# Kernel optimization log

Measured on AMD Instinct MI355X. Metric: run time of the kernel, lower is better.

The kernel has to match this reference:

```python
import math
import jax, jax.numpy as jnp
from jax import lax
import numpy as np

L, B, S, H, N = 2, 1, 2048, 1024, 16
HN = H // N
EPS = 1e-5
SIGMA = 0.02
OUT_STD = SIGMA / math.sqrt(2.0 * L)


def gelu(x):
    # OpenAI tanh-approx gelu, matching gelu_impl
    return 0.5 * x * (1.0 + jnp.tanh(0.7978845608028654 * x * (1.0 + 0.044715 * x * x)))


def layer_norm(x, g, b):
    mu = jnp.mean(x, axis=-1, keepdims=True)
    var = jnp.mean(jnp.square(x - mu), axis=-1, keepdims=True)
    return (x - mu) / jnp.sqrt(var + EPS) * g + b


def setup_inputs() -> dict:
    key = jax.random.key(0)
    ks = jax.random.split(key, 8)
    x = jax.random.normal(ks[0], (B, S, H), dtype=jnp.float32)
    ltor_mask = jnp.tril(jnp.ones((S, S), dtype=jnp.float32))[None, None]  # [1,1,S,S]
    return {
        "hidden_states": x,
        "ltor_mask": ltor_mask,
        "ln1_g": jnp.ones((L, H), jnp.float32),
        "ln1_b": jnp.zeros((L, H), jnp.float32),
        "qkv_w": jax.random.normal(ks[1], (L, H, 3 * H), jnp.float32) * SIGMA,
        "qkv_b": jnp.zeros((L, 3 * H), jnp.float32),
        "dense_w": jax.random.normal(ks[2], (L, H, H), jnp.float32) * OUT_STD,
        "dense_b": jnp.zeros((L, H), jnp.float32),
        "ln2_g": jnp.ones((L, H), jnp.float32),
        "ln2_b": jnp.zeros((L, H), jnp.float32),
        "fc_w": jax.random.normal(ks[3], (L, H, 4 * H), jnp.float32) * SIGMA,
        "fc_b": jnp.zeros((L, 4 * H), jnp.float32),
        "proj_w": jax.random.normal(ks[4], (L, 4 * H, H), jnp.float32) * OUT_STD,
        "proj_b": jnp.zeros((L, H), jnp.float32),
        "lnf_g": jnp.ones((H,), jnp.float32),
        "lnf_b": jnp.zeros((H,), jnp.float32),
    }


def _transformer(hidden_states, ltor_mask, ln1_g, ln1_b, qkv_w, qkv_b, dense_w, dense_b,
                 ln2_g, ln2_b, fc_w, fc_b, proj_w, proj_b, lnf_g, lnf_b):
    scale = 1.0 / math.sqrt(HN)

    def step(h, p):
        g1, b1, qw, qb, dw, db, g2, b2, fw, fb, pw, pb = p
        y = layer_norm(h, g1, b1)
        qkv = y @ qw + qb                       # [B,S,3H]
        q, k, v = jnp.split(qkv, 3, axis=-1)
        # [B,S,H] -> [B,N,S,HN]
        q = q.reshape(B, S, N, HN).transpose(0, 2, 1, 3)
        k = k.reshape(B, S, N, HN).transpose(0, 2, 1, 3)
        v = v.reshape(B, S, N, HN).transpose(0, 2, 1, 3)
        scores = jnp.einsum('bnqd,bnkd->bnqk', q, k) * scale
        scores = scores * ltor_mask - 10000.0 * (1.0 - ltor_mask)
        probs = jax.nn.softmax(scores, axis=-1)
        ctx = jnp.einsum('bnqk,bnkd->bnqd', probs, v)
        ctx = ctx.transpose(0, 2, 1, 3).reshape(B, S, H)
        attn_out = ctx @ dw + db
        h2 = h + attn_out
        y2 = layer_norm(h2, g2, b2)
        mlp_out = gelu(y2 @ fw + fb) @ pw + pb
        return h2 + mlp_out, None

    params = (ln1_g, ln1_b, qkv_w, qkv_b, dense_w, dense_b,
              ln2_g, ln2_b, fc_w, fc_b, proj_w, proj_b)
    h, _ = lax.scan(step, hidden_states, params)
    return layer_norm(h, lnf_g, lnf_b)


def reference(hidden_states, ltor_mask, ln1_g, ln1_b, qkv_w, qkv_b, dense_w, dense_b,
              ln2_g, ln2_b, fc_w, fc_b, proj_w, proj_b, lnf_g, lnf_b):
    return _transformer(hidden_states, ltor_mask, ln1_g, ln1_b, qkv_w, qkv_b,
                        dense_w, dense_b, ln2_g, ln2_b, fc_w, fc_b,
                        proj_w, proj_b, lnf_g, lnf_b)
```

## Files before the change

kernel.cpp:

```cpp
#include <hip/hip_runtime.h>
#include <hip/hip_bf16.h>
#include <cstdint>
#include <cstddef>

typedef __bf16 bf16;
typedef __attribute__((ext_vector_type(4))) __bf16 bf16x4;
typedef __attribute__((ext_vector_type(8))) __bf16 bf16x8;
typedef __attribute__((ext_vector_type(4))) float floatx4;

__device__ __forceinline__ void gload16(const bf16* g, bf16* l) {
    __builtin_amdgcn_global_load_lds(
        (const __attribute__((address_space(1))) void*)g,
        (__attribute__((address_space(3))) void*)l, 16, 0, 0);
}

__global__ __launch_bounds__(256) void ln_first(const float* __restrict__ x,
                                                float* __restrict__ h,
                                                const float* __restrict__ g,
                                                const float* __restrict__ b,
                                                bf16* __restrict__ y) {
    __shared__ float red[8];
    const int row = blockIdx.x, tid = threadIdx.x;
    const size_t off = (size_t)row * 1024 + tid * 4;
    const float4 v = *(const float4*)(x + off);
    *(float4*)(h + off) = v;
    float s = v.x + v.y + v.z + v.w;
#pragma unroll
    for (int o = 32; o > 0; o >>= 1) s += __shfl_xor(s, o);
    if ((tid & 63) == 0) red[tid >> 6] = s;
    __syncthreads();
    const float mean = (red[0] + red[1] + red[2] + red[3]) * (1.f / 1024.f);
    const float d[4] = {v.x - mean, v.y - mean, v.z - mean, v.w - mean};
    float q = d[0] * d[0] + d[1] * d[1] + d[2] * d[2] + d[3] * d[3];
#pragma unroll
    for (int o = 32; o > 0; o >>= 1) q += __shfl_xor(q, o);
    if ((tid & 63) == 0) red[4 + (tid >> 6)] = q;
    __syncthreads();
    const float var = (red[4] + red[5] + red[6] + red[7]) * (1.f / 1024.f);
    const float rstd = rsqrtf(var + 1e-5f);
    const int base = tid * 4;
#pragma unroll
    for (int i = 0; i < 4; i++)
        y[off + i] = (bf16)(d[i] * rstd * g[base + i] + b[base + i]);
}

template <typename OutT, int KS>
__global__ __launch_bounds__(256) void reduce_ln(const bf16* __restrict__ part,
                                                 const float* __restrict__ bias,
                                                 float* __restrict__ h,
                                                 const float* __restrict__ g,
                                                 const float* __restrict__ b,
                                                 OutT* __restrict__ y) {
    __shared__ float red[8];
    const int row = blockIdx.x, tid = threadIdx.x;
    const int base = tid * 4;
    const size_t off = (size_t)row * 1024 + base;
    const float4 hv = *(const float4*)(h + off);
    const float4 bv = *(const float4*)(bias + base);
    float a[4] = {hv.x + bv.x, hv.y + bv.y, hv.z + bv.z, hv.w + bv.w};
#pragma unroll
    for (int z = 0; z < KS; z++) {
        bf16x4 pv = *(const bf16x4*)(part + (size_t)z * (2048 * 1024) + off);
#pragma unroll
        for (int i = 0; i < 4; i++) a[i] += (float)pv[i];
    }
    *(float4*)(h + off) = (float4){a[0], a[1], a[2], a[3]};
    float s = a[0] + a[1] + a[2] + a[3];
#pragma unroll
    for (int o = 32; o > 0; o >>= 1) s += __shfl_xor(s, o);
    if ((tid & 63) == 0) red[tid >> 6] = s;
    __syncthreads();
    const float mean = (red[0] + red[1] + red[2] + red[3]) * (1.f / 1024.f);
    const float d[4] = {a[0] - mean, a[1] - mean, a[2] - mean, a[3] - mean};
    float q = d[0] * d[0] + d[1] * d[1] + d[2] * d[2] + d[3] * d[3];
#pragma unroll
    for (int o = 32; o > 0; o >>= 1) q += __shfl_xor(q, o);
    if ((tid & 63) == 0) red[4 + (tid >> 6)] = q;
    __syncthreads();
    const float var = (red[4] + red[5] + red[6] + red[7]) * (1.f / 1024.f);
    const float rstd = rsqrtf(var + 1e-5f);
#pragma unroll
    for (int i = 0; i < 4; i++)
        y[off + i] = (OutT)(d[i] * rstd * g[base + i] + b[base + i]);
}

__global__ __launch_bounds__(256) void transpose_cvt(const float* __restrict__ in,
                                                     bf16* __restrict__ out, int K, int N) {
    __shared__ float T[64][65];
    const int k0 = blockIdx.x * 64, n0 = blockIdx.y * 64;
    {
        const int r = threadIdx.x >> 4;
        const int c4 = (threadIdx.x & 15) * 4;
#pragma unroll
        for (int j = 0; j < 4; j++) {
            float4 v = *(const float4*)&in[(size_t)(k0 + r + j * 16) * N + n0 + c4];
            T[r + j * 16][c4 + 0] = v.x; T[r + j * 16][c4 + 1] = v.y;
            T[r + j * 16][c4 + 2] = v.z; T[r + j * 16][c4 + 3] = v.w;
        }
    }
    __syncthreads();
    {
        const int rn = threadIdx.x >> 3;
        const int c8 = (threadIdx.x & 7) * 8;
#pragma unroll
        for (int j = 0; j < 2; j++) {
            bf16x8 v;
#pragma unroll
            for (int i = 0; i < 8; i++) v[i] = (bf16)T[c8 + i][rn + j * 32];
            *(bf16x8*)&out[(size_t)(n0 + rn + j * 32) * K + k0 + c8] = v;
        }
    }
}

template <int MODE>
__global__ __launch_bounds__(256) void gemm_bt64(const bf16* __restrict__ A,
                                                 const bf16* __restrict__ BT,
                                                 const float* __restrict__ bias,
                                                 bf16* __restrict__ outb,
                                                 int M, int N, int K) {
    __shared__ bf16 As[64 * 64];
    __shared__ bf16 Bs[128 * 64];
    const int tid = threadIdx.x;
    const int w = tid >> 6, lane = tid & 63;
    const int quad = lane >> 4, l16 = lane & 15;
    const int wm = w >> 1, wn = w & 1;
    const int m0 = blockIdx.x * 64, n0 = blockIdx.y * 128;
    const int kchunk = K / gridDim.z;
    const int kbeg = blockIdx.z * kchunk;

    const int srow = lane >> 3;
    const int scol = ((lane & 7) ^ srow) * 8;
    const bf16* ga = A + (size_t)(m0 + w * 16 + srow) * K + kbeg + scol;
    const bf16* gb = BT + (size_t)(n0 + w * 32 + srow) * K + kbeg + scol;
    bf16* la = As + (w * 16) * 64;
    bf16* lb = Bs + (w * 32) * 64;

    floatx4 acc[2][4];
#pragma unroll
    for (int i = 0; i < 2; i++)
#pragma unroll
        for (int j = 0; j < 4; j++) acc[i][j] = (floatx4){0.f, 0.f, 0.f, 0.f};

#pragma unroll
    for (int s = 0; s < 2; s++) gload16(ga + (size_t)(s * 8) * K, la + s * 8 * 64);
#pragma unroll
    for (int s = 0; s < 4; s++) gload16(gb + (size_t)(s * 8) * K, lb + s * 8 * 64);

    const int xq = (l16 & 7) * 8;

    for (int kk = 0; kk < kchunk; kk += 64) {
        __syncthreads();
        bf16x8 af[2][2], bfr[2][4];
#pragma unroll
        for (int ks = 0; ks < 2; ks++) {
            const int colz = (ks * 32 + quad * 8) ^ xq;
#pragma unroll
            for (int i = 0; i < 2; i++)
                af[ks][i]  = *(const bf16x8*)&As[(wm * 32 + i * 16 + l16) * 64 + colz];
#pragma unroll
            for (int i = 0; i < 4; i++)
                bfr[ks][i] = *(const bf16x8*)&Bs[(wn * 64 + i * 16 + l16) * 64 + colz];
        }
        __syncthreads();
        if (kk + 64 < kchunk) {
#pragma unroll
            for (int s = 0; s < 2; s++) gload16(ga + (size_t)(s * 8) * K + kk + 64, la + s * 8 * 64);
#pragma unroll
            for (int s = 0; s < 4; s++) gload16(gb + (size_t)(s * 8) * K + kk + 64, lb + s * 8 * 64);
        }
#pragma unroll
        for (int ks = 0; ks < 2; ks++)
#pragma unroll
            for (int ms = 0; ms < 2; ms++)
#pragma unroll
                for (int ns = 0; ns < 4; ns++)
                    acc[ms][ns] = __builtin_amdgcn_mfma_f32_16x16x32_bf16(af[ks][ms], bfr[ks][ns],
                                                                          acc[ms][ns], 0, 0, 0);
    }

    bf16* pout = (MODE == 2) ? (outb + (size_t)blockIdx.z * M * N) : outb;
#pragma unroll
    for (int ms = 0; ms < 2; ms++) {
#pragma unroll
        for (int ns = 0; ns < 4; ns++) {
            const int row = m0 + wm * 32 + ms * 16 + quad * 4;
            const int col = n0 + wn * 64 + ns * 16 + l16;
            const float bv = (MODE == 2) ? 0.f : bias[col];
#pragma unroll
            for (int i = 0; i < 4; i++) {
                float v = acc[ms][ns][i] + bv;
                size_t idx = (size_t)(row + i) * N + col;
                if (MODE == 1) {
                    float t = 0.7978845608028654f * v * (1.f + 0.044715f * v * v);
                    pout[idx] = (bf16)(0.5f * v * (1.f + tanhf(t)));
                } else {
                    pout[idx] = (bf16)v;
                }
            }
        }
    }
}

__global__ __launch_bounds__(256) void attn_mfma(const bf16* __restrict__ qkv,
                                                 bf16* __restrict__ ctx) {
    __shared__ bf16 Ks[64][68];
    __shared__ bf16 Vt[64][72];
    __shared__ bf16 QPa[64][68];
    __shared__ bf16 QPb[64][68];
    const int tid = threadIdx.x;
    const int w = tid >> 6, lane = tid & 63;
    const int quad = lane >> 4, l16 = lane & 15;
    const int head = blockIdx.y;
    const int qta = blockIdx.x;
    const int qtb = 31 - qta;
    const int qa = qta * 64, qb = qtb * 64;
    const int rowg = w * 16 + quad * 4;
    const int r = tid >> 2;
    const int c = (tid & 3) * 16;
    const float SC = 0.18033688011111827f;

    {
        const bf16* pa = qkv + (size_t)(qa + r) * 3072 + head * 64 + c;
        const bf16* pb = qkv + (size_t)(qb + r) * 3072 + head * 64 + c;
        bf16x8 a0 = *(const bf16x8*)pa, a1 = *(const bf16x8*)(pa + 8);
        bf16x8 b0 = *(const bf16x8*)pb, b1 = *(const bf16x8*)(pb + 8);
        bf16x8 sa0, sa1, sb0, sb1;
#pragma unroll
        for (int i = 0; i < 8; i++) {
            sa0[i] = (bf16)((float)a0[i] * SC); sa1[i] = (bf16)((float)a1[i] * SC);
            sb0[i] = (bf16)((float)b0[i] * SC); sb1[i] = (bf16)((float)b1[i] * SC);
        }
        *(bf16x8*)&QPa[r][c] = sa0; *(bf16x8*)&QPa[r][c + 8] = sa1;
        *(bf16x8*)&QPb[r][c] = sb0; *(bf16x8*)&QPb[r][c + 8] = sb1;
    }
    const bf16x8 aqA0 = *(const bf16x8*)&QPa[w * 16 + l16][quad * 8];
    const bf16x8 aqA1 = *(const bf16x8*)&QPa[w * 16 + l16][32 + quad * 8];
    const bf16x8 aqB0 = *(const bf16x8*)&QPb[w * 16 + l16][quad * 8];
    const bf16x8 aqB1 = *(const bf16x8*)&QPb[w * 16 + l16][32 + quad * 8];

    float lsa[4] = {0.f, 0.f, 0.f, 0.f}, lsb[4] = {0.f, 0.f, 0.f, 0.f};
    floatx4 oa[4], ob[4];
#pragma unroll
    for (int d = 0; d < 4; d++) {
        oa[d] = (floatx4){0.f, 0.f, 0.f, 0.f};
        ob[d] = (floatx4){0.f, 0.f, 0.f, 0.f};
    }

    const int nt = qtb + 1;
    bf16x8 kr0, kr1, vr0, vr1;
    {
        const bf16* kp = qkv + (size_t)r * 3072 + 1024 + head * 64 + c;
        kr0 = *(const bf16x8*)kp; kr1 = *(const bf16x8*)(kp + 8);
        const bf16* vp = qkv + (size_t)lane * 3072 + 2048 + head * 64 + w * 16;
        vr0 = *(const bf16x8*)vp; vr1 = *(const bf16x8*)(vp + 8);
    }

    for (int t = 0; t < nt; t++) {
        __syncthreads();
        *(bf16x8*)&Ks[r][c] = kr0;
        *(bf16x8*)&Ks[r][c + 8] = kr1;
#pragma unroll
        for (int i = 0; i < 8; i++) {
            Vt[w * 16 + i][lane] = vr0[i];
            Vt[w * 16 + 8 + i][lane] = vr1[i];
        }
        __syncthreads();
        if (t + 1 < nt) {
            const size_t kb = (size_t)(t + 1) * 64;
            const bf16* kp = qkv + (kb + r) * 3072 + 1024 + head * 64 + c;
            kr0 = *(const bf16x8*)kp; kr1 = *(const bf16x8*)(kp + 8);
            const bf16* vp = qkv + (kb + lane) * 3072 + 2048 + head * 64 + w * 16;
            vr0 = *(const bf16x8*)vp; vr1 = *(const bf16x8*)(vp + 8);
        }
        const bool doA = (t <= qta);

        floatx4 s4b[4], s4a[4];
#pragma unroll
        for (int n = 0; n < 4; n++) s4b[n] = (floatx4){0.f, 0.f, 0.f, 0.f};
#pragma unroll
        for (int n = 0; n < 4; n++) {
            bf16x8 bk0 = *(const bf16x8*)&Ks[n * 16 + l16][quad * 8];
            bf16x8 bk1 = *(const bf16x8*)&Ks[n * 16 + l16][32 + quad * 8];
            s4b[n] = __builtin_amdgcn_mfma_f32_16x16x32_bf16(aqB0, bk0, s4b[n], 0, 0, 0);
            s4b[n] = __builtin_amdgcn_mfma_f32_16x16x32_bf16(aqB1, bk1, s4b[n], 0, 0, 0);
        }
        if (doA) {
#pragma unroll
            for (int n = 0; n < 4; n++) s4a[n] = (floatx4){0.f, 0.f, 0.f, 0.f};
#pragma unroll
            for (int n = 0; n < 4; n++) {
                bf16x8 bk0 = *(const bf16x8*)&Ks[n * 16 + l16][quad * 8];
                bf16x8 bk1 = *(const bf16x8*)&Ks[n * 16 + l16][32 + quad * 8];
                s4a[n] = __builtin_amdgcn_mfma_f32_16x16x32_bf16(aqA0, bk0, s4a[n], 0, 0, 0);
                s4a[n] = __builtin_amdgcn_mfma_f32_16x16x32_bf16(aqA1, bk1, s4a[n], 0, 0, 0);
            }
        }

        {
            float p[4][4];
            if (t == nt - 1) {
#pragma unroll
                for (int i = 0; i < 4; i++)
#pragma unroll
                    for (int n = 0; n < 4; n++)
                        p[n][i] = (n * 16 + l16 > rowg + i) ? 0.f
                                  : __builtin_amdgcn_exp2f(s4b[n][i]);
            } else {
#pragma unroll
                for (int i = 0; i < 4; i++)
#pragma unroll
                    for (int n = 0; n < 4; n++)
                        p[n][i] = __builtin_amdgcn_exp2f(s4b[n][i]);
            }
#pragma unroll
            for (int i = 0; i < 4; i++)
#pragma unroll
                for (int n = 0; n < 4; n++) lsb[i] += p[n][i];
#pragma unroll
            for (int n = 0; n < 4; n++)
#pragma unroll
                for (int i = 0; i < 4; i++)
                    QPb[rowg + i][n * 16 + l16] = (bf16)p[n][i];
        }
        if (doA) {
            float p[4][4];
            if (t == qta) {
#pragma unroll
                for (int i = 0; i < 4; i++)
#pragma unroll
                    for (int n = 0; n < 4; n++)
                        p[n][i] = (n * 16 + l16 > rowg + i) ? 0.f
                                  : __builtin_amdgcn_exp2f(s4a[n][i]);
            } else {
#pragma unroll
                for (int i = 0; i < 4; i++)
#pragma unroll
                    for (int n = 0; n < 4; n++)
                        p[n][i] = __builtin_amdgcn_exp2f(s4a[n][i]);
            }
#pragma unroll
            for (int i = 0; i < 4; i++)
#pragma unroll
                for (int n = 0; n < 4; n++) lsa[i] += p[n][i];
#pragma unroll
            for (int n = 0; n < 4; n++)
#pragma unroll
                for (int i = 0; i < 4; i++)
                    QPa[rowg + i][n * 16 + l16] = (bf16)p[n][i];
        }

        {
            bf16x8 ap0 = *(const bf16x8*)&QPb[w * 16 + l16][quad * 8];
            bf16x8 ap1 = *(const bf16x8*)&QPb[w * 16 + l16][32 + quad * 8];
#pragma unroll
            for (int d = 0; d < 4; d++) {
                bf16x8 bv0 = *(const bf16x8*)&Vt[d * 16 + l16][quad * 8];
                bf16x8 bv1 = *(const bf16x8*)&Vt[d * 16 + l16][32 + quad * 8];
                ob[d] = __builtin_amdgcn_mfma_f32_16x16x32_bf16(ap0, bv0, ob[d], 0, 0, 0);
                ob[d] = __builtin_amdgcn_mfma_f32_16x16x32_bf16(ap1, bv1, ob[d], 0, 0, 0);
            }
        }
        if (doA) {
            bf16x8 ap0 = *(const bf16x8*)&QPa[w * 16 + l16][quad * 8];
            bf16x8 ap1 = *(const bf16x8*)&QPa[w * 16 + l16][32 + quad * 8];
#pragma unroll
            for (int d = 0; d < 4; d++) {
                bf16x8 bv0 = *(const bf16x8*)&Vt[d * 16 + l16][quad * 8];
                bf16x8 bv1 = *(const bf16x8*)&Vt[d * 16 + l16][32 + quad * 8];
                oa[d] = __builtin_amdgcn_mfma_f32_16x16x32_bf16(ap0, bv0, oa[d], 0, 0, 0);
                oa[d] = __builtin_amdgcn_mfma_f32_16x16x32_bf16(ap1, bv1, oa[d], 0, 0, 0);
            }
        }
    }

#pragma unroll
    for (int i = 0; i < 4; i++) {
#pragma unroll
        for (int msk = 1; msk < 16; msk <<= 1) {
            lsb[i] += __shfl_xor(lsb[i], msk);
            lsa[i] += __shfl_xor(lsa[i], msk);
        }
    }
#pragma unroll
    for (int i = 0; i < 4; i++) {
        const float rlb = 1.f / lsb[i];
        const float rla = 1.f / lsa[i];
        const size_t rbB = (size_t)(qb + rowg + i) * 1024 + head * 64;
        const size_t rbA = (size_t)(qa + rowg + i) * 1024 + head * 64;
#pragma unroll
        for (int d = 0; d < 4; d++) {
            ctx[rbB + d * 16 + l16] = (bf16)(ob[d][i] * rlb);
            ctx[rbA + d * 16 + l16] = (bf16)(oa[d][i] * rla);
        }
    }
}

extern "C" void kernel_launch(void* const* d_in, const int* in_sizes, int n_in,
                              void* d_out, int out_size, void* d_ws, size_t ws_size,
                              hipStream_t stream) {
    const float* hidden  = (const float*)d_in[0];
    const float* ln1_g   = (const float*)d_in[2];
    const float* ln1_b   = (const float*)d_in[3];
    const float* qkv_w   = (const float*)d_in[4];
    const float* qkv_b   = (const float*)d_in[5];
    const float* dense_w = (const float*)d_in[6];
    const float* dense_b = (const float*)d_in[7];
    const float* ln2_g   = (const float*)d_in[8];
    const float* ln2_b   = (const float*)d_in[9];
    const float* fc_w    = (const float*)d_in[10];
    const float* fc_b    = (const float*)d_in[11];
    const float* proj_w  = (const float*)d_in[12];
    const float* proj_b  = (const float*)d_in[13];
    const float* lnf_g   = (const float*)d_in[14];
    const float* lnf_b   = (const float*)d_in[15];

    char* ws = (char*)d_ws;
    float* h   = (float*)(ws);
    bf16* y    = (bf16*)(ws + 8u  * 1024 * 1024);
    bf16* qkv  = (bf16*)(ws + 12u * 1024 * 1024);
    bf16* ctx  = (bf16*)(ws + 24u * 1024 * 1024);
    bf16* mlp  = (bf16*)(ws + 12u * 1024 * 1024);
    bf16* wT   = (bf16*)(ws + 28u * 1024 * 1024);
    bf16* part = (bf16*)(ws + 36u * 1024 * 1024);

    ln_first<<<2048, 256, 0, stream>>>(hidden, h, ln1_g, ln1_b, y);

    for (int l = 0; l < 2; l++) {
        transpose_cvt<<<dim3(16, 48), 256, 0, stream>>>(qkv_w + (size_t)l * 1024 * 3072, wT, 1024, 3072);
        gemm_bt64<0><<<dim3(32, 24, 1), 256, 0, stream>>>(y, wT, qkv_b + l * 3072, qkv, 2048, 3072, 1024);

        attn_mfma<<<dim3(16, 16), 256, 0, stream>>>(qkv, ctx);

        transpose_cvt<<<dim3(16, 16), 256, 0, stream>>>(dense_w + (size_t)l * 1024 * 1024, wT, 1024, 1024);
        gemm_bt64<2><<<dim3(32, 8, 4), 256, 0, stream>>>(ctx, wT, nullptr, part, 2048, 1024, 1024);
        reduce_ln<bf16, 4><<<2048, 256, 0, stream>>>(part, dense_b + l * 1024, h,
                                                     ln2_g + l * 1024, ln2_b + l * 1024, y);

        transpose_cvt<<<dim3(16, 64), 256, 0, stream>>>(fc_w + (size_t)l * 1024 * 4096, wT, 1024, 4096);
        gemm_bt64<1><<<dim3(32, 32, 1), 256, 0, stream>>>(y, wT, fc_b + l * 4096, mlp, 2048, 4096, 1024);

        transpose_cvt<<<dim3(64, 16), 256, 0, stream>>>(proj_w + (size_t)l * 4096 * 1024, wT, 4096, 1024);
        gemm_bt64<2><<<dim3(32, 8, 4), 256, 0, stream>>>(mlp, wT, nullptr, part, 2048, 1024, 4096);
        if (l == 0) {
            reduce_ln<bf16, 4><<<2048, 256, 0, stream>>>(part, proj_b, h,
                                                         ln1_g + 1024, ln1_b + 1024, y);
        } else {
            reduce_ln<float, 4><<<2048, 256, 0, stream>>>(part, proj_b + 1024, h,
                                                          lnf_g, lnf_b, (float*)d_out);
        }
    }
}
```

Measured before the change: 447.8 us.

## Split attention KV range across two blocks and batch weight transposes into one launch

The attention kernel now launches twice as many blocks. Each paired query tile's long causal row range is split in two: one block handles the first half of the KV tiles together with the short tile, the other handles the rest. The split partial outputs and row sums go to float scratch and a new combine kernel merges them. The intent is to use more CUs, since the old grid of 256 blocks underfilled the GPU. Separately, the eight per-layer weight transpose launches are merged into a single launch that writes both layers' bf16 transposed weights up front, removing launch gaps. The cost is extra scratch traffic, one extra kernel launch per layer, and a larger workspace.

New measurement: 452.7 us. Within noise of the previous version (+1.1%).

```diff
diff --git a/kernel.cpp b/kernel.cpp
--- a/kernel.cpp
+++ b/kernel.cpp
@@ -84,16 +84,28 @@
         y[off + i] = (OutT)(d[i] * rstd * g[base + i] + b[base + i]);
 }
 
-__global__ __launch_bounds__(256) void transpose_cvt(const float* __restrict__ in,
-                                                     bf16* __restrict__ out, int K, int N) {
+__global__ __launch_bounds__(256) void transpose_all(const float* __restrict__ qkv_w,
+                                                     const float* __restrict__ dense_w,
+                                                     const float* __restrict__ fc_w,
+                                                     const float* __restrict__ proj_w,
+                                                     bf16* __restrict__ wT) {
     __shared__ float T[64][65];
-    const int k0 = blockIdx.x * 64, n0 = blockIdx.y * 64;
+    int b = blockIdx.x;
+    const int layer = (b >= 3072) ? 1 : 0;
+    b -= layer * 3072;
+    const float* src; bf16* dst; int K, N, kx, ny;
+    bf16* wl = wT + (size_t)layer * 12582912;
+    if (b < 768)       { src = qkv_w  + (size_t)layer * 1024 * 3072; dst = wl;            K = 1024; N = 3072; kx = b & 15; ny = b >> 4; }
+    else if (b < 1024) { b -= 768;  src = dense_w + (size_t)layer * 1024 * 1024; dst = wl + 3145728; K = 1024; N = 1024; kx = b & 15; ny = b >> 4; }
+    else if (b < 2048) { b -= 1024; src = fc_w   + (size_t)layer * 1024 * 4096; dst = wl + 4194304; K = 1024; N = 4096; kx = b & 15; ny = b >> 4; }
+    else               { b -= 2048; src = proj_w + (size_t)layer * 4096 * 1024; dst = wl + 8388608; K = 4096; N = 1024; kx = b & 63; ny = b >> 6; }
+    const int k0 = kx * 64, n0 = ny * 64;
     {
         const int r = threadIdx.x >> 4;
         const int c4 = (threadIdx.x & 15) * 4;
 #pragma unroll
         for (int j = 0; j < 4; j++) {
-            float4 v = *(const float4*)&in[(size_t)(k0 + r + j * 16) * N + n0 + c4];
+            float4 v = *(const float4*)&src[(size_t)(k0 + r + j * 16) * N + n0 + c4];
             T[r + j * 16][c4 + 0] = v.x; T[r + j * 16][c4 + 1] = v.y;
             T[r + j * 16][c4 + 2] = v.z; T[r + j * 16][c4 + 3] = v.w;
         }
@@ -107,7 +119,7 @@
             bf16x8 v;
 #pragma unroll
             for (int i = 0; i < 8; i++) v[i] = (bf16)T[c8 + i][rn + j * 32];
-            *(bf16x8*)&out[(size_t)(n0 + rn + j * 32) * K + k0 + c8] = v;
+            *(bf16x8*)&dst[(size_t)(n0 + rn + j * 32) * K + k0 + c8] = v;
         }
     }
 }
@@ -202,7 +214,9 @@
 }
 
 __global__ __launch_bounds__(256) void attn_mfma(const bf16* __restrict__ qkv,
-                                                 bf16* __restrict__ ctx) {
+                                                 bf16* __restrict__ ctx,
+                                                 float* __restrict__ po,
+                                                 float* __restrict__ pls) {
     __shared__ bf16 Ks[64][68];
     __shared__ bf16 Vt[64][72];
     __shared__ bf16 QPa[64][68];
@@ -211,32 +225,47 @@
     const int w = tid >> 6, lane = tid & 63;
     const int quad = lane >> 4, l16 = lane & 15;
     const int head = blockIdx.y;
-    const int qta = blockIdx.x;
-    const int qtb = 31 - qta;
+    const int bx = blockIdx.x;
+    const int type = bx >> 4;
+    const int p = bx & 15;
+    const int qta = p, qtb = 31 - p;
     const int qa = qta * 64, qb = qtb * 64;
+    const int slot = (head * 16 + (15 - p)) * 2 + type;
+    const int t0 = type ? (16 - p) : 0;
+    const int TendB0 = 16 - p;
+    const int Tend = type ? (32 - p) : ((p + 1 > TendB0) ? p + 1 : TendB0);
     const int rowg = w * 16 + quad * 4;
     const int r = tid >> 2;
     const int c = (tid & 3) * 16;
     const float SC = 0.18033688011111827f;
 
     {
-        const bf16* pa = qkv + (size_t)(qa + r) * 3072 + head * 64 + c;
         const bf16* pb = qkv + (size_t)(qb + r) * 3072 + head * 64 + c;
-        bf16x8 a0 = *(const bf16x8*)pa, a1 = *(const bf16x8*)(pa + 8);
         bf16x8 b0 = *(const bf16x8*)pb, b1 = *(const bf16x8*)(pb + 8);
-        bf16x8 sa0, sa1, sb0, sb1;
+        bf16x8 sb0, sb1;
 #pragma unroll
         for (int i = 0; i < 8; i++) {
-            sa0[i] = (bf16)((float)a0[i] * SC); sa1[i] = (bf16)((float)a1[i] * SC);
             sb0[i] = (bf16)((float)b0[i] * SC); sb1[i] = (bf16)((float)b1[i] * SC);
         }
-        *(bf16x8*)&QPa[r][c] = sa0; *(bf16x8*)&QPa[r][c + 8] = sa1;
         *(bf16x8*)&QPb[r][c] = sb0; *(bf16x8*)&QPb[r][c + 8] = sb1;
-    }
-    const bf16x8 aqA0 = *(const bf16x8*)&QPa[w * 16 + l16][quad * 8];
-    const bf16x8 aqA1 = *(const bf16x8*)&QPa[w * 16 + l16][32 + quad * 8];
+        if (type == 0) {
+            const bf16* pa = qkv + (size_t)(qa + r) * 3072 + head * 64 + c;
+            bf16x8 a0 = *(const bf16x8*)pa, a1 = *(const bf16x8*)(pa + 8);
+            bf16x8 sa0, sa1;
+#pragma unroll
+            for (int i = 0; i < 8; i++) {
+                sa0[i] = (bf16)((float)a0[i] * SC); sa1[i] = (bf16)((float)a1[i] * SC);
+            }
+            *(bf16x8*)&QPa[r][c] = sa0; *(bf16x8*)&QPa[r][c + 8] = sa1;
+        }
+    }
     const bf16x8 aqB0 = *(const bf16x8*)&QPb[w * 16 + l16][quad * 8];
     const bf16x8 aqB1 = *(const bf16x8*)&QPb[w * 16 + l16][32 + quad * 8];
+    bf16x8 aqA0{}, aqA1{};
+    if (type == 0) {
+        aqA0 = *(const bf16x8*)&QPa[w * 16 + l16][quad * 8];
+        aqA1 = *(const bf16x8*)&QPa[w * 16 + l16][32 + quad * 8];
+    }
 
     float lsa[4] = {0.f, 0.f, 0.f, 0.f}, lsb[4] = {0.f, 0.f, 0.f, 0.f};
     floatx4 oa[4], ob[4];
@@ -246,16 +275,15 @@
         ob[d] = (floatx4){0.f, 0.f, 0.f, 0.f};
     }
 
-    const int nt = qtb + 1;
     bf16x8 kr0, kr1, vr0, vr1;
     {
-        const bf16* kp = qkv + (size_t)r * 3072 + 1024 + head * 64 + c;
+        const bf16* kp = qkv + ((size_t)t0 * 64 + r) * 3072 + 1024 + head * 64 + c;
         kr0 = *(const bf16x8*)kp; kr1 = *(const bf16x8*)(kp + 8);
-        const bf16* vp = qkv + (size_t)lane * 3072 + 2048 + head * 64 + w * 16;
+        const bf16* vp = qkv + ((size_t)t0 * 64 + lane) * 3072 + 2048 + head * 64 + w * 16;
         vr0 = *(const bf16x8*)vp; vr1 = *(const bf16x8*)(vp + 8);
     }
 
-    for (int t = 0; t < nt; t++) {
+    for (int t = t0; t < Tend; t++) {
         __syncthreads();
         *(bf16x8*)&Ks[r][c] = kr0;
         *(bf16x8*)&Ks[r][c + 8] = kr1;
@@ -265,24 +293,27 @@
             Vt[w * 16 + 8 + i][lane] = vr1[i];
         }
         __syncthreads();
-        if (t + 1 < nt) {
+        if (t + 1 < Tend) {
             const size_t kb = (size_t)(t + 1) * 64;
             const bf16* kp = qkv + (kb + r) * 3072 + 1024 + head * 64 + c;
             kr0 = *(const bf16x8*)kp; kr1 = *(const bf16x8*)(kp + 8);
             const bf16* vp = qkv + (kb + lane) * 3072 + 2048 + head * 64 + w * 16;
             vr0 = *(const bf16x8*)vp; vr1 = *(const bf16x8*)(vp + 8);
         }
-        const bool doA = (t <= qta);
+        const bool doB = type ? true : (t < TendB0);
+        const bool doA = (type == 0) && (t <= qta);
 
         floatx4 s4b[4], s4a[4];
-#pragma unroll
-        for (int n = 0; n < 4; n++) s4b[n] = (floatx4){0.f, 0.f, 0.f, 0.f};
-#pragma unroll
-        for (int n = 0; n < 4; n++) {
-            bf16x8 bk0 = *(const bf16x8*)&Ks[n * 16 + l16][quad * 8];
-            bf16x8 bk1 = *(const bf16x8*)&Ks[n * 16 + l16][32 + quad * 8];
-            s4b[n] = __builtin_amdgcn_mfma_f32_16x16x32_bf16(aqB0, bk0, s4b[n], 0, 0, 0);
-            s4b[n] = __builtin_amdgcn_mfma_f32_16x16x32_bf16(aqB1, bk1, s4b[n], 0, 0, 0);
+        if (doB) {
+#pragma unroll
+            for (int n = 0; n < 4; n++) s4b[n] = (floatx4){0.f, 0.f, 0.f, 0.f};
+#pragma unroll
+            for (int n = 0; n < 4; n++) {
+                bf16x8 bk0 = *(const bf16x8*)&Ks[n * 16 + l16][quad * 8];
+                bf16x8 bk1 = *(const bf16x8*)&Ks[n * 16 + l16][32 + quad * 8];
+                s4b[n] = __builtin_amdgcn_mfma_f32_16x16x32_bf16(aqB0, bk0, s4b[n], 0, 0, 0);
+                s4b[n] = __builtin_amdgcn_mfma_f32_16x16x32_bf16(aqB1, bk1, s4b[n], 0, 0, 0);
+            }
         }
         if (doA) {
 #pragma unroll
@@ -296,60 +327,60 @@
             }
         }
 
-        {
-            float p[4][4];
-            if (t == nt - 1) {
+        if (doB) {
+            float p4[4][4];
+            if (t == qtb) {
 #pragma unroll
                 for (int i = 0; i < 4; i++)
 #pragma unroll
                     for (int n = 0; n < 4; n++)
-                        p[n][i] = (n * 16 + l16 > rowg + i) ? 0.f
-                                  : __builtin_amdgcn_exp2f(s4b[n][i]);
+                        p4[n][i] = (n * 16 + l16 > rowg + i) ? 0.f
+                                   : __builtin_amdgcn_exp2f(s4b[n][i]);
             } else {
 #pragma unroll
                 for (int i = 0; i < 4; i++)
 #pragma unroll
                     for (int n = 0; n < 4; n++)
-                        p[n][i] = __builtin_amdgcn_exp2f(s4b[n][i]);
+                        p4[n][i] = __builtin_amdgcn_exp2f(s4b[n][i]);
             }
 #pragma unroll
             for (int i = 0; i < 4; i++)
 #pragma unroll
-                for (int n = 0; n < 4; n++) lsb[i] += p[n][i];
+                for (int n = 0; n < 4; n++) lsb[i] += p4[n][i];
 #pragma unroll
             for (int n = 0; n < 4; n++)
 #pragma unroll
                 for (int i = 0; i < 4; i++)
-                    QPb[rowg + i][n * 16 + l16] = (bf16)p[n][i];
+                    QPb[rowg + i][n * 16 + l16] = (bf16)p4[n][i];
         }
         if (doA) {
-            float p[4][4];
+            float p4[4][4];
             if (t == qta) {
 #pragma unroll
                 for (int i = 0; i < 4; i++)
 #pragma unroll
                     for (int n = 0; n < 4; n++)
-                        p[n][i] = (n * 16 + l16 > rowg + i) ? 0.f
-                                  : __builtin_amdgcn_exp2f(s4a[n][i]);
+                        p4[n][i] = (n * 16 + l16 > rowg + i) ? 0.f
+                                   : __builtin_amdgcn_exp2f(s4a[n][i]);
             } else {
 #pragma unroll
                 for (int i = 0; i < 4; i++)
 #pragma unroll
                     for (int n = 0; n < 4; n++)
-                        p[n][i] = __builtin_amdgcn_exp2f(s4a[n][i]);
+                        p4[n][i] = __builtin_amdgcn_exp2f(s4a[n][i]);
             }
 #pragma unroll
             for (int i = 0; i < 4; i++)
 #pragma unroll
-                for (int n = 0; n < 4; n++) lsa[i] += p[n][i];
+                for (int n = 0; n < 4; n++) lsa[i] += p4[n][i];
 #pragma unroll
             for (int n = 0; n < 4; n++)
 #pragma unroll
                 for (int i = 0; i < 4; i++)
-                    QPa[rowg + i][n * 16 + l16] = (bf16)p[n][i];
-        }
-
-        {
+                    QPa[rowg + i][n * 16 + l16] = (bf16)p4[n][i];
+        }
+
+        if (doB) {
             bf16x8 ap0 = *(const bf16x8*)&QPb[w * 16 + l16][quad * 8];
             bf16x8 ap1 = *(const bf16x8*)&QPb[w * 16 + l16][32 + quad * 8];
 #pragma unroll
@@ -378,20 +409,52 @@
 #pragma unroll
         for (int msk = 1; msk < 16; msk <<= 1) {
             lsb[i] += __shfl_xor(lsb[i], msk);
-            lsa[i] += __shfl_xor(lsa[i], msk);
-        }
-    }
-#pragma unroll
-    for (int i = 0; i < 4; i++) {
-        const float rlb = 1.f / lsb[i];
-        const float rla = 1.f / lsa[i];
-        const size_t rbB = (size_t)(qb + rowg + i) * 1024 + head * 64;
-        const size_t rbA = (size_t)(qa + rowg + i) * 1024 + head * 64;
-#pragma unroll
-        for (int d = 0; d < 4; d++) {
-            ctx[rbB + d * 16 + l16] = (bf16)(ob[d][i] * rlb);
-            ctx[rbA + d * 16 + l16] = (bf16)(oa[d][i] * rla);
-        }
+            if (type == 0) lsa[i] += __shfl_xor(lsa[i], msk);
+        }
+    }
+    {
+        float* pob = po + (size_t)slot * 4096;
+#pragma unroll
+        for (int i = 0; i < 4; i++)
+#pragma unroll
+            for (int d = 0; d < 4; d++)
+                pob[(rowg + i) * 64 + d * 16 + l16] = ob[d][i];
+        if (l16 == 0) {
+#pragma unroll
+            for (int i = 0; i < 4; i++) pls[slot * 64 + rowg + i] = lsb[i];
+        }
+    }
+    if (type == 0) {
+#pragma unroll
+        for (int i = 0; i < 4; i++) {
+            const float rla = 1.f / lsa[i];
+            const size_t rbA = (size_t)(qa + rowg + i) * 1024 + head * 64;
+#pragma unroll
+            for (int d = 0; d < 4; d++)
+                ctx[rbA + d * 16 + l16] = (bf16)(oa[d][i] * rla);
+        }
+    }
+}
+
+__global__ __launch_bounds__(256) void attn_combine(const float* __restrict__ po,
+                                                    const float* __restrict__ pls,
+                                                    bf16* __restrict__ ctx) {
+    const int hs = blockIdx.x;
+    const int head = hs >> 4, s = hs & 15;
+    const int tid = threadIdx.x;
+    const int row = tid >> 2, c0 = (tid & 3) * 16;
+    const float rls = 1.f / (pls[(hs * 2 + 0) * 64 + row] + pls[(hs * 2 + 1) * 64 + row]);
+    const float* p0 = po + (size_t)(hs * 2 + 0) * 4096 + row * 64 + c0;
+    const float* p1 = po + (size_t)(hs * 2 + 1) * 4096 + row * 64 + c0;
+    bf16* out = ctx + (size_t)((16 + s) * 64 + row) * 1024 + head * 64 + c0;
+#pragma unroll
+    for (int j = 0; j < 4; j++) {
+        const float4 a = *(const float4*)(p0 + j * 4);
+        const float4 b = *(const float4*)(p1 + j * 4);
+        out[j * 4 + 0] = (bf16)((a.x + b.x) * rls);
+        out[j * 4 + 1] = (bf16)((a.y + b.y) * rls);
+        out[j * 4 + 2] = (bf16)((a.z + b.z) * rls);
+        out[j * 4 + 3] = (bf16)((a.w + b.w) * rls);
     }
 }
 
@@ -415,32 +478,37 @@
     const float* lnf_b   = (const float*)d_in[15];
 
     char* ws = (char*)d_ws;
-    float* h   = (float*)(ws);
-    bf16* y    = (bf16*)(ws + 8u  * 1024 * 1024);
-    bf16* qkv  = (bf16*)(ws + 12u * 1024 * 1024);
-    bf16* ctx  = (bf16*)(ws + 24u * 1024 * 1024);
-    bf16* mlp  = (bf16*)(ws + 12u * 1024 * 1024);
-    bf16* wT   = (bf16*)(ws + 28u * 1024 * 1024);
-    bf16* part = (bf16*)(ws + 36u * 1024 * 1024);
-
+    float* h    = (float*)(ws);
+    bf16* y     = (bf16*)(ws + 8u   * 1024 * 1024);
+    bf16* qkvb  = (bf16*)(ws + 12u  * 1024 * 1024);
+    bf16* ctx   = (bf16*)(ws + 24u  * 1024 * 1024);
+    bf16* mlp   = (bf16*)(ws + 12u  * 1024 * 1024);
+    bf16* part  = (bf16*)(ws + 36u  * 1024 * 1024);
+    bf16* wT    = (bf16*)(ws + 52u  * 1024 * 1024);
+    float* po   = (float*)(ws + 104u * 1024 * 1024);
+    float* pls  = (float*)(ws + 114u * 1024 * 1024);
+
+    const size_t LW = 12582912;
+
+    transpose_all<<<6144, 256, 0, stream>>>(qkv_w, dense_w, fc_w, proj_w, wT);
     ln_first<<<2048, 256, 0, stream>>>(hidden, h, ln1_g, ln1_b, y);
 
     for (int l = 0; l < 2; l++) {
-        transpose_cvt<<<dim3(16, 48), 256, 0, stream>>>(qkv_w + (size_t)l * 1024 * 3072, wT, 1024, 3072);
-        gemm_bt64<0><<<dim3(32, 24, 1), 256, 0, stream>>>(y, wT, qkv_b + l * 3072, qkv, 2048, 3072, 1024);
-
-        attn_mfma<<<dim3(16, 16), 256, 0, stream>>>(qkv, ctx);
-
-        transpose_cvt<<<dim3(16, 16), 256, 0, stream>>>(dense_w + (size_t)l * 1024 * 1024, wT, 1024, 1024);
-        gemm_bt64<2><<<dim3(32, 8, 4), 256, 0, stream>>>(ctx, wT, nullptr, part, 2048, 1024, 1024);
+        bf16* wTq = wT + (size_t)l * LW;
+        bf16* wTd = wTq + 3145728;
+        bf16* wTf = wTq + 4194304;
+        bf16* wTp = wTq + 8388608;
+
+        gemm_bt64<0><<<dim3(32, 24, 1), 256, 0, stream>>>(y, wTq, qkv_b + l * 3072, qkvb, 2048, 3072, 1024);
+        attn_mfma<<<dim3(32, 16), 256, 0, stream>>>(qkvb, ctx, po, pls);
+        attn_combine<<<256, 256, 0, stream>>>(po, pls, ctx);
+
+        gemm_bt64<2><<<dim3(32, 8, 4), 256, 0, stream>>>(ctx, wTd, nullptr, part, 2048, 1024, 1024);
         reduce_ln<bf16, 4><<<2048, 256, 0, stream>>>(part, dense_b + l * 1024, h,
                                                      ln2_g + l * 1024, ln2_b + l * 1024, y);
 
-        transpose_cvt<<<dim3(16, 64), 256, 0, stream>>>(fc_w + (size_t)l * 1024 * 4096, wT, 1024, 4096);
-        gemm_bt64<1><<<dim3(32, 32, 1), 256, 0, stream>>>(y, wT, fc_b + l * 4096, mlp, 2048, 4096, 1024);
-
-        transpose_cvt<<<dim3(64, 16), 256, 0, stream>>>(proj_w + (size_t)l * 4096 * 1024, wT, 4096, 1024);
-        gemm_bt64<2><<<dim3(32, 8, 4), 256, 0, stream>>>(mlp, wT, nullptr, part, 2048, 1024, 4096);
+        gemm_bt64<1><<<dim3(32, 32, 1), 256, 0, stream>>>(y, wTf, fc_b + l * 4096, mlp, 2048, 4096, 1024);
+        gemm_bt64<2><<<dim3(32, 8, 4), 256, 0, stream>>>(mlp, wTp, nullptr, part, 2048, 1024, 4096);
         if (l == 0) {
             reduce_ln<bf16, 4><<<2048, 256, 0, stream>>>(part, proj_b, h,
                                                          ln1_g + 1024, ln1_b + 1024, y);
```
